# Performance work log

Measured on AMD Instinct MI355X. Metric: run time of the kernel, lower is better.

The kernel has to match this reference:

```python
import jax, jax.numpy as jnp
import numpy as np

B, L, D = 64, 512, 768

def setup_inputs() -> dict:
    key = jax.random.key(0)
    k1, k2, k3, k4 = jax.random.split(key, 4)
    hidden_states = jax.random.normal(k1, (B, L, D), dtype=jnp.float32)
    # nn.Linear(hidden_size, hidden_size): weight [D, D], bias [D]
    W = jax.random.normal(k2, (D, D), dtype=jnp.float32) * (1.0 / np.sqrt(D))
    b = jax.random.normal(k3, (D,), dtype=jnp.float32) * 0.02
    # context_vector: [D, 1]
    context_vector = jax.random.normal(k4, (D, 1), dtype=jnp.float32)
    return {"hidden_states": hidden_states, "W": W, "b": b, "context_vector": context_vector}

def reference(hidden_states, W, b, context_vector):
    # tanh(dense(h)): [B, L, D]; torch Linear uses x @ W.T + b
    proj = jnp.tanh(jnp.einsum('bld,ed->ble', hidden_states, W) + b)
    # scores: [B, L]
    scores = jnp.einsum('bld,d->bl', proj, context_vector[:, 0])
    # softmax over sequence dim (dim=1)
    attention_weights = jax.nn.softmax(scores, axis=1)
    # weighted sum over sequence: [B, D]
    weighted_output = jnp.einsum('bld,bl->bd', hidden_states, attention_weights)
    return (weighted_output, attention_weights)
```

## Files before the change

### kernel.cpp

```cpp
#include <hip/hip_runtime.h>
#include <hip/hip_bf16.h>


using half8 = __attribute__((ext_vector_type(8))) _Float16;
using f32x4 = __attribute__((ext_vector_type(4))) float;

#define AS1 __attribute__((address_space(1)))
#define AS3 __attribute__((address_space(3)))

__device__ __forceinline__ void gload_lds16(const void* g, void* l) {
  __builtin_amdgcn_global_load_lds((const AS1 void*)g, (AS3 void*)l, 16, 0, 0);
}

__device__ __forceinline__ unsigned short f2h(float x) {
  _Float16 h = (_Float16)x;
  return __builtin_bit_cast(unsigned short, h);
}

__device__ __forceinline__ float tanh_fast(float x) {
  return 1.0f - __fdividef(2.0f, 1.0f + __expf(2.0f * x));
}

__global__ void convert_w(const float4* __restrict__ W4, ushort4* __restrict__ Wt) {
  int i = blockIdx.x * 256 + threadIdx.x;
  float4 x = W4[i];
  ushort4 o;
  o.x = f2h(x.x); o.y = f2h(x.y); o.z = f2h(x.z); o.w = f2h(x.w);
  Wt[i] = o;
}

__global__ __launch_bounds__(256) void gemm_scores(
    const float* __restrict__ H, const ushort* __restrict__ Wt,
    const float* __restrict__ bias, const float* __restrict__ cvec,
    float* __restrict__ part) {
  __shared__ float  ldsAlo[2][2048];
  __shared__ float  ldsAhi[2][2048];
  __shared__ ushort ldsB[2][4096];
  __shared__ float scpart[2][128];

  const int tid = threadIdx.x;
  const int lane = tid & 63;
  const int wid = tid >> 6;
  const int wr = wid >> 1, wc = wid & 1;
  const int m = lane & 15, q = lane >> 4;

  const int bid = blockIdx.x;
  const int xcd = bid & 7;
  const int slot = bid >> 3;
  const int mtile = xcd * 32 + slot / 6;
  const int ntile = slot % 6;

  const char* const Abase = (const char*)(H + (size_t)(mtile * 128) * 768);
  const char* const Bbase = (const char*)Wt + (size_t)(ntile * 128) * 1536;

  const int tr3 = tid >> 3;
  const int au = (tid & 7) ^ (tr3 & 7);
  const size_t asrcLO = (size_t)((au >> 2) * 64 + tr3) * 3072 + (au & 3) * 32;

  const int up = au;
  const size_t bsrc0 = (size_t)((up >> 2) * 64 + tr3) * 1536 + (up & 3) * 16;
  const size_t bsrc1 = (size_t)((up >> 2) * 64 + 32 + tr3) * 1536 + (up & 3) * 16;
  const int wavebase = wid << 10;

  f32x4 acc[4][4];
  #pragma unroll
  for (int i = 0; i < 4; ++i)
    #pragma unroll
    for (int j = 0; j < 4; ++j)
      acc[i][j] = (f32x4){0.f, 0.f, 0.f, 0.f};

  auto stage = [&](int kt, int s) {
    #pragma unroll
    for (int c = 0; c < 2; ++c) {
      const char* srcLO = Abase + asrcLO + (size_t)c * 98304 + kt * 128;
      gload_lds16(srcLO,      (char*)ldsAlo[s] + c * 4096 + wavebase);
      gload_lds16(srcLO + 16, (char*)ldsAhi[s] + c * 4096 + wavebase);
    }
    gload_lds16(Bbase + bsrc0 + kt * 64, (char*)ldsB[s] + wavebase);
    gload_lds16(Bbase + bsrc1 + kt * 64, (char*)ldsB[s] + 4096 + wavebase);
  };

  const int aslot = ((wr * 4 + q) ^ (m & 7)) * 16;
  const int bslot = ((wc * 4 + q) ^ (m & 7)) * 16;

  auto compute = [&](int s) {
    const char* AbLO = (const char*)ldsAlo[s];
    const char* AbHI = (const char*)ldsAhi[s];
    const char* Bb = (const char*)ldsB[s];
    half8 areg[4], breg[4];
    #pragma unroll
    for (int mi = 0; mi < 4; ++mi) {
      int rowb = (mi * 16 + m) * 128;
      f32x4 lo = *(const f32x4*)(AbLO + rowb + aslot);
      f32x4 hi = *(const f32x4*)(AbHI + rowb + aslot);
      half8 r;
      r[0] = (_Float16)lo[0]; r[1] = (_Float16)lo[1];
      r[2] = (_Float16)lo[2]; r[3] = (_Float16)lo[3];
      r[4] = (_Float16)hi[0]; r[5] = (_Float16)hi[1];
      r[6] = (_Float16)hi[2]; r[7] = (_Float16)hi[3];
      areg[mi] = r;
    }
    #pragma unroll
    for (int ni = 0; ni < 4; ++ni)
      breg[ni] = *(const half8*)(Bb + (ni * 16 + m) * 128 + bslot);
    __builtin_amdgcn_s_setprio(1);
    #pragma unroll
    for (int mi = 0; mi < 4; ++mi)
      #pragma unroll
      for (int ni = 0; ni < 4; ++ni)
        acc[mi][ni] = __builtin_amdgcn_mfma_f32_16x16x32_f16(
            areg[mi], breg[ni], acc[mi][ni], 0, 0, 0);
    __builtin_amdgcn_s_setprio(0);
  };

  stage(0, 0);
  __syncthreads();
  #pragma unroll
  for (int t = 0; t < 24; ++t) {
    if (t < 23) stage(t + 1, (t + 1) & 1);
    compute(t & 1);
    __syncthreads();
  }

  float bb[4], cc[4];
  #pragma unroll
  for (int ni = 0; ni < 4; ++ni) {
    int e = ntile * 128 + wc * 64 + ni * 16 + m;
    bb[ni] = bias[e];
    cc[ni] = cvec[e];
  }
  #pragma unroll
  for (int mi = 0; mi < 4; ++mi) {
    #pragma unroll
    for (int j = 0; j < 4; ++j) {
      float s = 0.f;
      #pragma unroll
      for (int ni = 0; ni < 4; ++ni)
        s += tanh_fast(acc[mi][ni][j] + bb[ni]) * cc[ni];
      s += __shfl_xor(s, 1);
      s += __shfl_xor(s, 2);
      s += __shfl_xor(s, 4);
      s += __shfl_xor(s, 8);
      if (m == 0) scpart[wc][wr * 64 + mi * 16 + q * 4 + j] = s;
    }
  }
  __syncthreads();
  if (tid < 128)
    part[ntile * 32768 + mtile * 128 + tid] = scpart[0][tid] + scpart[1][tid];
}


__global__ void wsum_fused(const float* __restrict__ H, const float* __restrict__ prt,
                           float* __restrict__ out) {
  int b = blockIdx.x, dc = blockIdx.y;
  int t = threadIdx.x;
  __shared__ float w[512];
  __shared__ float redm[2], reds[2];

  float s[4];
  #pragma unroll
  for (int i = 0; i < 4; ++i) {
    int r = b * 512 + t + i * 128;
    s[i] = prt[r] + prt[32768 + r] + prt[2 * 32768 + r] +
           prt[3 * 32768 + r] + prt[4 * 32768 + r] + prt[5 * 32768 + r];
  }
  float mx = fmaxf(fmaxf(s[0], s[1]), fmaxf(s[2], s[3]));
  #pragma unroll
  for (int o = 32; o >= 1; o >>= 1) mx = fmaxf(mx, __shfl_xor(mx, o));
  if ((t & 63) == 0) redm[t >> 6] = mx;
  __syncthreads();
  mx = fmaxf(redm[0], redm[1]);

  float e[4], sm = 0.f;
  #pragma unroll
  for (int i = 0; i < 4; ++i) { e[i] = __expf(s[i] - mx); sm += e[i]; }
  #pragma unroll
  for (int o = 32; o >= 1; o >>= 1) sm += __shfl_xor(sm, o);
  if ((t & 63) == 0) reds[t >> 6] = sm;
  __syncthreads();
  float inv = 1.0f / (reds[0] + reds[1]);
  #pragma unroll
  for (int i = 0; i < 4; ++i) w[t + i * 128] = e[i] * inv;
  __syncthreads();

  int d0 = dc * 256 + t * 2;
  const float2* hp = (const float2*)(H + (size_t)b * 512 * 768 + d0);
  float a0 = 0.f, a1 = 0.f;
  #pragma unroll 8
  for (int l = 0; l < 512; ++l) {
    float2 u = hp[(size_t)l * 384];
    float wl = w[l];
    a0 += wl * u.x;
    a1 += wl * u.y;
  }
  out[b * 768 + d0] = a0;
  out[b * 768 + d0 + 1] = a1;

  if (dc == 0) {
    #pragma unroll
    for (int i = 0; i < 4; ++i)
      out[49152 + b * 512 + t + i * 128] = w[t + i * 128];
  }
}

extern "C" void kernel_launch(void* const* d_in, const int* in_sizes, int n_in,
                              void* d_out, int out_size, void* d_ws, size_t ws_size,
                              hipStream_t stream) {
  const float* H    = (const float*)d_in[0];
  const float* W    = (const float*)d_in[1];
  const float* bias = (const float*)d_in[2];
  const float* cvec = (const float*)d_in[3];
  float* out = (float*)d_out;

  char* ws = (char*)d_ws;
  ushort* Wt = (ushort*)(ws + 0);
  float*  prt = (float*)(ws + 1179648);

  hipLaunchKernelGGL(convert_w, dim3(576), dim3(256), 0, stream,
                     (const float4*)W, (ushort4*)Wt);
  hipLaunchKernelGGL(gemm_scores, dim3(1536), dim3(256), 0, stream,
                     H, Wt, bias, cvec, prt);
  hipLaunchKernelGGL(wsum_fused, dim3(64, 3), dim3(128), 0, stream,
                     H, prt, out);
}
```

Measured before the change: 105.7 us.

## Emit fp16 copy of H from GEMM and read it in weighted sum

Result: no change. 105.5 us (-0.2%).

```diff
diff --git a/kernel.cpp b/kernel.cpp
--- a/kernel.cpp
+++ b/kernel.cpp
@@ -32,7 +32,7 @@
 __global__ __launch_bounds__(256) void gemm_scores(
     const float* __restrict__ H, const ushort* __restrict__ Wt,
     const float* __restrict__ bias, const float* __restrict__ cvec,
-    float* __restrict__ part) {
+    float* __restrict__ part, ushort* __restrict__ Ah) {
   __shared__ float  ldsAlo[2][2048];
   __shared__ float  ldsAhi[2][2048];
   __shared__ ushort ldsB[2][4096];
@@ -57,9 +57,8 @@
   const int au = (tid & 7) ^ (tr3 & 7);
   const size_t asrcLO = (size_t)((au >> 2) * 64 + tr3) * 3072 + (au & 3) * 32;
 
-  const int up = au;
-  const size_t bsrc0 = (size_t)((up >> 2) * 64 + tr3) * 1536 + (up & 3) * 16;
-  const size_t bsrc1 = (size_t)((up >> 2) * 64 + 32 + tr3) * 1536 + (up & 3) * 16;
+  const size_t bsrc0 = (size_t)((au >> 2) * 64 + tr3) * 1536 + (au & 3) * 16;
+  const size_t bsrc1 = (size_t)((au >> 2) * 64 + 32 + tr3) * 1536 + (au & 3) * 16;
   const int wavebase = wid << 10;
 
   f32x4 acc[4][4];
@@ -83,7 +82,9 @@
   const int aslot = ((wr * 4 + q) ^ (m & 7)) * 16;
   const int bslot = ((wc * 4 + q) ^ (m & 7)) * 16;
 
-  auto compute = [&](int s) {
+  ushort* const ahbase = Ah + (size_t)(mtile * 128 + wr * 64 + m) * 768 + q * 8;
+
+  auto compute = [&](int s, int t) {
     const char* AbLO = (const char*)ldsAlo[s];
     const char* AbHI = (const char*)ldsAhi[s];
     const char* Bb = (const char*)ldsB[s];
@@ -100,6 +101,11 @@
       r[6] = (_Float16)hi[2]; r[7] = (_Float16)hi[3];
       areg[mi] = r;
     }
+    if ((t % 6) == ntile && wc == 0) {
+      #pragma unroll
+      for (int mi = 0; mi < 4; ++mi)
+        *(half8*)(ahbase + (size_t)(mi * 16) * 768 + t * 32) = areg[mi];
+    }
     #pragma unroll
     for (int ni = 0; ni < 4; ++ni)
       breg[ni] = *(const half8*)(Bb + (ni * 16 + m) * 128 + bslot);
@@ -118,7 +124,7 @@
   #pragma unroll
   for (int t = 0; t < 24; ++t) {
     if (t < 23) stage(t + 1, (t + 1) & 1);
-    compute(t & 1);
+    compute(t & 1, t);
     __syncthreads();
   }
 
@@ -149,8 +155,7 @@
     part[ntile * 32768 + mtile * 128 + tid] = scpart[0][tid] + scpart[1][tid];
 }
 
-
-__global__ void wsum_fused(const float* __restrict__ H, const float* __restrict__ prt,
+__global__ void wsum_fused(const ushort* __restrict__ Ah, const float* __restrict__ prt,
                            float* __restrict__ out) {
   int b = blockIdx.x, dc = blockIdx.y;
   int t = threadIdx.x;
@@ -184,14 +189,14 @@
   __syncthreads();
 
   int d0 = dc * 256 + t * 2;
-  const float2* hp = (const float2*)(H + (size_t)b * 512 * 768 + d0);
+  const ushort* hp = Ah + (size_t)b * 512 * 768 + d0;
   float a0 = 0.f, a1 = 0.f;
   #pragma unroll 8
   for (int l = 0; l < 512; ++l) {
-    float2 u = hp[(size_t)l * 384];
+    unsigned u = *(const unsigned*)(hp + (size_t)l * 768);
     float wl = w[l];
-    a0 += wl * u.x;
-    a1 += wl * u.y;
+    a0 += wl * (float)__builtin_bit_cast(_Float16, (unsigned short)(u & 0xffff));
+    a1 += wl * (float)__builtin_bit_cast(_Float16, (unsigned short)(u >> 16));
   }
   out[b * 768 + d0] = a0;
   out[b * 768 + d0 + 1] = a1;
@@ -215,11 +220,12 @@
   char* ws = (char*)d_ws;
   ushort* Wt = (ushort*)(ws + 0);
   float*  prt = (float*)(ws + 1179648);
+  ushort* Ah = (ushort*)(ws + 1966080);
 
   hipLaunchKernelGGL(convert_w, dim3(576), dim3(256), 0, stream,
                      (const float4*)W, (ushort4*)Wt);
   hipLaunchKernelGGL(gemm_scores, dim3(1536), dim3(256), 0, stream,
-                     H, Wt, bias, cvec, prt);
+                     H, Wt, bias, cvec, prt, Ah);
   hipLaunchKernelGGL(wsum_fused, dim3(64, 3), dim3(128), 0, stream,
-                     H, prt, out);
-}
+                     Ah, prt, out);
+}
```
